# Kernel optimization log

Measured on AMD Instinct MI355X. Metric: run time of the kernel, lower is better.

The kernel has to match this reference:

```python
import jax, jax.numpy as jnp
import numpy as np

B, S, C = 4, 2048, 2048
D = C // 4  # head dim = 512

def setup_inputs() -> dict:
    key = jax.random.key(0)
    k1, k2, k3, k4, k5 = jax.random.split(key, 5)
    scale = 1.0 / np.sqrt(C)
    return {
        "x": jax.random.normal(k1, (B, S, C), dtype=jnp.float32),
        "Wqkv": jax.random.normal(k2, (3 * D, C), dtype=jnp.float32) * scale,
        "bqkv": jax.random.normal(k3, (3 * D,), dtype=jnp.float32) * 0.01,
        "Wo": jax.random.normal(k4, (C, D), dtype=jnp.float32) * (1.0 / np.sqrt(D)),
        "bo": jax.random.normal(k5, (C,), dtype=jnp.float32) * 0.01,
    }

def reference(x, Wqkv, bqkv, Wo, bo):
    Bx, Sx, Cx = x.shape
    d = Cx // 4
    # fused QKV projection: [B,S,3d] -> split into q,k,v each [B,S,d]
    qkv = jnp.einsum('bsc,oc->bso', x, Wqkv) + bqkv
    qkv = qkv.reshape(Bx, Sx, 3, d)
    q, k, v = qkv[:, :, 0], qkv[:, :, 1], qkv[:, :, 2]
    # scaled dot-product attention (full [B,S,S] scores, as in original)
    attn = jnp.einsum('bqd,bkd->bqk', q, k) / jnp.sqrt(jnp.asarray(d, x.dtype))
    attn = jax.nn.softmax(attn, axis=-1)
    ctx = jnp.einsum('bqk,bkd->bqd', attn, v)
    # output projection d -> C
    return jnp.einsum('bsd,od->bso', ctx, Wo) + bo
```

## Files before the change

kernel.cpp:

```cpp
#include <hip/hip_runtime.h>
#include <math.h>


typedef __bf16 bf16;
typedef bf16 bf16x8 __attribute__((ext_vector_type(8)));
typedef bf16 bf16x4 __attribute__((ext_vector_type(4)));
typedef float f32x4 __attribute__((ext_vector_type(4)));

#define BB 4
#define SS 2048
#define CC 2048
#define DD 512
#define ND3 1536
#define MM 8192

typedef const __attribute__((address_space(1))) unsigned int g_u32;
typedef __attribute__((address_space(3))) unsigned int l_u32;

__device__ __forceinline__ void gl_lds16(const bf16* g, bf16* l) {
    __builtin_amdgcn_global_load_lds((g_u32*)g, (l_u32*)l, 16, 0, 0);
}

#define N4_X   (MM * CC / 4)
#define N4_WQ  (ND3 * CC / 4)
#define N4_WO  (CC * DD / 4)
#define N4_RS  (MM / 4)
#define N4_TOT (N4_X + N4_WQ + N4_WO + N4_RS)

__global__ __launch_bounds__(256) void prep(const float* __restrict__ x,
                                            const float* __restrict__ Wqkv,
                                            const float* __restrict__ Wo,
                                            bf16* __restrict__ xb,
                                            bf16* __restrict__ wqkvb,
                                            bf16* __restrict__ wob,
                                            float* __restrict__ rsum) {
    int i = blockIdx.x * 256 + threadIdx.x;
    const int stride = gridDim.x * 256;
    for (; i < N4_TOT; i += stride) {
        if (i < N4_X + N4_WQ + N4_WO) {
            const float* src; bf16* dst; int j = i;
            if (j < N4_X)                { src = x;    dst = xb; }
            else if (j < N4_X + N4_WQ)   { src = Wqkv; dst = wqkvb; j -= N4_X; }
            else                         { src = Wo;   dst = wob;   j -= N4_X + N4_WQ; }
            float4 v = ((const float4*)src)[j];
            bf16x4 o;
            o[0] = (bf16)v.x; o[1] = (bf16)v.y; o[2] = (bf16)v.z; o[3] = (bf16)v.w;
            ((bf16x4*)dst)[j] = o;
        } else {
            int j = i - (N4_X + N4_WQ + N4_WO);
            ((float4*)rsum)[j] = float4{0.f, 0.f, 0.f, 0.f};
        }
    }
}

#define SLOT_E 16384
#define CH_B   8192

template <bool OUT_BF16, int EPI>
__device__ __forceinline__ void gemm256_body(const bf16* __restrict__ A,
                                             const bf16* __restrict__ Bm,
                                             const float* __restrict__ bias,
                                             float* __restrict__ rowsum,
                                             bf16* __restrict__ vTp,
                                             void* __restrict__ Cv,
                                             int K, int lda, int ldb, int ldc,
                                             long ab, long bb, long cb,
                                             float scale) {
    extern __shared__ bf16 lds[];
    A  += (size_t)blockIdx.z * ab;
    Bm += (size_t)blockIdx.z * bb;
    const int m0 = blockIdx.y * 256, n0 = blockIdx.x * 256;
    const int t = threadIdx.x, lane = t & 63, w = t >> 6;
    const int wm = (w >> 2) * 128, wn = (w & 3) * 64;
    const int cl = lane & 15, q = lane >> 4;
    const int swzr = (q ^ ((cl >> 1) & 3)) * 8;
    const int srow = t >> 2;
    const int swz  = (t & 3) ^ ((t >> 3) & 3);
    const bf16* pa = A  + (size_t)(m0 + srow) * lda + swz * 8;
    const bf16* pb = Bm + (size_t)(n0 + srow) * ldb + swz * 8;
    bf16* lw = lds + w * 512;

    f32x4 acc[8][4] = {};
    const int NC = K >> 5;

    auto STAGE = [&](int j) {
        bf16* s = lw + (j & 3) * SLOT_E;
        const bf16* ga = pa + j * 32;
        const bf16* gb = pb + j * 32;
        gl_lds16(ga,                     s);
        gl_lds16(ga + (size_t)128 * lda, s + 4096);
        gl_lds16(gb,                     s + CH_B);
        gl_lds16(gb + (size_t)128 * ldb, s + CH_B + 4096);
    };
    auto FRAGS = [&](int j, bf16x8 (&af)[8], bf16x8 (&bfr)[4]) {
        const bf16* sa = lds + (j & 3) * SLOT_E + (wm + cl) * 32 + swzr;
        const bf16* sb = lds + (j & 3) * SLOT_E + CH_B + (wn + cl) * 32 + swzr;
#pragma unroll
        for (int i = 0; i < 8; i++)  af[i]  = *(const bf16x8*)(sa + i * 512);
#pragma unroll
        for (int jj = 0; jj < 4; jj++) bfr[jj] = *(const bf16x8*)(sb + jj * 512);
    };
    auto MFMAS = [&](bf16x8 (&af)[8], bf16x8 (&bfr)[4]) {
        __builtin_amdgcn_s_setprio(1);
#pragma unroll
        for (int i = 0; i < 8; i++)
#pragma unroll
            for (int jj = 0; jj < 4; jj++)
                acc[i][jj] = __builtin_amdgcn_mfma_f32_16x16x32_bf16(
                                 af[i], bfr[jj], acc[i][jj], 0, 0, 0);
        __builtin_amdgcn_s_setprio(0);
    };

    STAGE(0); STAGE(1); STAGE(2);
    asm volatile("s_waitcnt vmcnt(8)" ::: "memory");
    __builtin_amdgcn_s_barrier();

    for (int j = 0; j < NC - 3; ++j) {
        bf16x8 af[8], bfr[4];
        FRAGS(j, af, bfr);
        STAGE(j + 3);
        MFMAS(af, bfr);
        asm volatile("s_waitcnt vmcnt(8)" ::: "memory");
        __builtin_amdgcn_s_barrier();
    }
    {   bf16x8 af[8], bfr[4];
        FRAGS(NC - 3, af, bfr); MFMAS(af, bfr);
        asm volatile("s_waitcnt vmcnt(4)" ::: "memory");
        __builtin_amdgcn_s_barrier();
    }
    {   bf16x8 af[8], bfr[4];
        FRAGS(NC - 2, af, bfr); MFMAS(af, bfr);
        asm volatile("s_waitcnt vmcnt(0)" ::: "memory");
        __builtin_amdgcn_s_barrier();
    }
    {   bf16x8 af[8], bfr[4];
        FRAGS(NC - 1, af, bfr); MFMAS(af, bfr);
    }

    if constexpr (EPI == 4) {
        float cs[4] = {0.f, 0.f, 0.f, 0.f};
#pragma unroll
        for (int i = 0; i < 8; i++)
#pragma unroll
            for (int jj = 0; jj < 4; jj++) {
                int col = n0 + wn + jj * 16 + cl;
                int row = m0 + wm + i * 16 + q * 4;
                bf16x4 o;
#pragma unroll
                for (int r = 0; r < 4; r++) {
                    float e = __expf(acc[i][jj][r] * scale);
                    cs[jj] += e;
                    o[r] = (bf16)e;
                }
                *(bf16x4*)&((bf16*)Cv)[(size_t)blockIdx.z * cb + (size_t)col * ldc + row] = o;
            }
#pragma unroll
        for (int jj = 0; jj < 4; jj++) {
            cs[jj] += __shfl_xor(cs[jj], 16, 64);
            cs[jj] += __shfl_xor(cs[jj], 32, 64);
        }
        if (q == 0) {
#pragma unroll
            for (int jj = 0; jj < 4; jj++)
                atomicAdd(&rowsum[(size_t)blockIdx.z * SS + n0 + wn + jj * 16 + cl], cs[jj]);
        }
        return;
    }

    const bool v_block = (EPI == 3) && (n0 >= 1024);
#pragma unroll
    for (int i = 0; i < 8; i++) {
#pragma unroll
        for (int jj = 0; jj < 4; jj++) {
            int col = n0 + wn + jj * 16 + cl;
            float bvv = bias ? bias[col] : 0.0f;
            if (v_block) {
                int row = m0 + wm + i * 16 + q * 4;
                int b = row >> 11, s = row & 2047;
                bf16x4 o;
#pragma unroll
                for (int r = 0; r < 4; r++) o[r] = (bf16)(acc[i][jj][r] * scale + bvv);
                *(bf16x4*)&vTp[((size_t)b * DD + (col - 1024)) * SS + s] = o;
            } else {
#pragma unroll
                for (int r = 0; r < 4; r++) {
                    int row = m0 + wm + i * 16 + q * 4 + r;
                    float val = acc[i][jj][r] * scale + bvv;
                    if (OUT_BF16)
                        ((bf16*)Cv)[(size_t)blockIdx.z * cb + (size_t)row * ldc + col] = (bf16)val;
                    else
                        ((float*)Cv)[(size_t)blockIdx.z * cb + (size_t)row * ldc + col] = val;
                }
            }
        }
    }
}

template <bool OUT_BF16, int BN, int EPI>
__device__ __forceinline__ void gemm_body(const bf16* __restrict__ A,
                                          const bf16* __restrict__ Bm,
                                          const float* __restrict__ bias,
                                          float* __restrict__ rowsum,
                                          bf16* __restrict__ vTp,
                                          void* __restrict__ Cv,
                                          int K, int lda, int ldb, int ldc,
                                          long ab, long bb, long cb,
                                          float scale) {
    constexpr int TM = (BN == 128) ? 4 : 2;
    constexpr int NB = (BN == 128) ? 4 : 2;
    __shared__ bf16 As[128 * 64];
    __shared__ bf16 Bs[BN * 64];
    A += (size_t)blockIdx.z * ab;
    Bm += (size_t)blockIdx.z * bb;
    const int m0 = blockIdx.y * 128, n0 = blockIdx.x * BN;
    const int t = threadIdx.x, lane = t & 63, w = t >> 6;
    const int wm = (BN == 128) ? (w >> 1) * 64 : w * 32;
    const int wn = (BN == 128) ? (w & 1) * 64 : 0;
    const int q = lane >> 4, cl = lane & 15;
    const int srow = lane >> 3;
    const int sblk = (lane & 7) ^ srow;
    const int scol = sblk * 8;
    const bf16* pa = A + (size_t)(m0 + w * 32 + srow) * lda + scol;
    const int brow0 = (BN == 128) ? w * 32 : w * 16;
    const bf16* pb = Bm + (size_t)(n0 + brow0 + srow) * ldb + scol;
    bf16* lA = As + (w * 32) * 64;
    bf16* lB = Bs + brow0 * 64;
    const int rblk0 = (q ^ (cl & 7)) * 8;
    const int rblk1 = ((4 + q) ^ (cl & 7)) * 8;

    f32x4 acc[TM][4] = {};
    for (int k0 = 0; k0 < K; k0 += 64) {
#pragma unroll
        for (int n = 0; n < 4; n++)
            gl_lds16(pa + k0 + (size_t)(n * 8) * lda, lA + n * 8 * 64);
#pragma unroll
        for (int n = 0; n < NB; n++)
            gl_lds16(pb + k0 + (size_t)(n * 8) * ldb, lB + n * 8 * 64);
        __syncthreads();
#pragma unroll
        for (int h = 0; h < 2; h++) {
            const int rb = h ? rblk1 : rblk0;
            bf16x8 af[TM], bfr[4];
#pragma unroll
            for (int i = 0; i < TM; i++)
                af[i] = *(const bf16x8*)&As[(wm + i * 16 + cl) * 64 + rb];
#pragma unroll
            for (int j = 0; j < 4; j++)
                bfr[j] = *(const bf16x8*)&Bs[(wn + j * 16 + cl) * 64 + rb];
#pragma unroll
            for (int i = 0; i < TM; i++)
#pragma unroll
                for (int j = 0; j < 4; j++)
                    acc[i][j] = __builtin_amdgcn_mfma_f32_16x16x32_bf16(af[i], bfr[j], acc[i][j], 0, 0, 0);
        }
        __syncthreads();
    }

    if constexpr (EPI == 4 || EPI == 5) {
        float inv[4], cs[4] = {0.f, 0.f, 0.f, 0.f};
        if constexpr (EPI == 5) {
#pragma unroll
            for (int j = 0; j < 4; j++)
                inv[j] = 1.0f / rowsum[(size_t)blockIdx.z * SS + n0 + wn + j * 16 + cl];
        }
#pragma unroll
        for (int i = 0; i < TM; i++)
#pragma unroll
            for (int j = 0; j < 4; j++) {
                int col = n0 + wn + j * 16 + cl;
                int row = m0 + wm + i * 16 + q * 4;
                bf16x4 o;
                if constexpr (EPI == 4) {
#pragma unroll
                    for (int r = 0; r < 4; r++) {
                        float e = __expf(acc[i][j][r] * scale);
                        cs[j] += e;
                        o[r] = (bf16)e;
                    }
                } else {
#pragma unroll
                    for (int r = 0; r < 4; r++) o[r] = (bf16)(acc[i][j][r] * inv[j]);
                }
                *(bf16x4*)&((bf16*)Cv)[(size_t)blockIdx.z * cb + (size_t)col * ldc + row] = o;
            }
        if constexpr (EPI == 4) {
#pragma unroll
            for (int j = 0; j < 4; j++) {
                cs[j] += __shfl_xor(cs[j], 16, 64);
                cs[j] += __shfl_xor(cs[j], 32, 64);
            }
            if (q == 0) {
#pragma unroll
                for (int j = 0; j < 4; j++)
                    atomicAdd(&rowsum[(size_t)blockIdx.z * SS + n0 + wn + j * 16 + cl], cs[j]);
            }
        }
        return;
    }
}

__global__ __launch_bounds__(512, 2) void k_qkv(const bf16* A, const bf16* Bm,
        const float* bias, bf16* vTp, void* Cv, int K, int lda, int ldb, int ldc,
        float scale) {
    gemm256_body<true, 3>(A, Bm, bias, nullptr, vTp, Cv, K, lda, ldb, ldc, 0, 0, 0, scale);
}
__global__ __launch_bounds__(512, 2) void k_score(const bf16* A, const bf16* Bm,
        float* rowsum, void* Cv, int K, int lda, int ldb, int ldc,
        long ab, long bb, long cb, float scale) {
    gemm256_body<true, 4>(A, Bm, nullptr, rowsum, nullptr, Cv, K, lda, ldb, ldc, ab, bb, cb, scale);
}
__global__ __launch_bounds__(256) void k_pv(const bf16* A, const bf16* Bm,
        float* rowsum, void* Cv, int K, int lda, int ldb, int ldc,
        long ab, long bb, long cb, float scale) {
    gemm_body<true, 64, 5>(A, Bm, nullptr, rowsum, nullptr, Cv, K, lda, ldb, ldc, ab, bb, cb, scale);
}
__global__ __launch_bounds__(512, 2) void k_out(const bf16* A, const bf16* Bm,
        const float* bias, void* Cv, int K, int lda, int ldb, int ldc,
        float scale) {
    gemm256_body<false, 0>(A, Bm, bias, nullptr, nullptr, Cv, K, lda, ldb, ldc, 0, 0, 0, scale);
}

extern "C" void kernel_launch(void* const* d_in, const int* in_sizes, int n_in,
                              void* d_out, int out_size, void* d_ws, size_t ws_size,
                              hipStream_t stream) {
    const float* x    = (const float*)d_in[0];
    const float* Wqkv = (const float*)d_in[1];
    const float* bqkv = (const float*)d_in[2];
    const float* Wo   = (const float*)d_in[3];
    const float* bo   = (const float*)d_in[4];
    float* out = (float*)d_out;

    char* ws = (char*)d_ws;
    size_t off = 0;
    bf16* xb    = (bf16*)(ws + off); off += (size_t)MM * CC * 2;
    bf16* wqkvb = (bf16*)(ws + off); off += (size_t)ND3 * CC * 2;
    bf16* wob   = (bf16*)(ws + off); off += (size_t)CC * DD * 2;
    bf16* qkvb  = (bf16*)(ws + off); off += (size_t)MM * ND3 * 2;
    bf16* vT    = (bf16*)(ws + off); off += (size_t)BB * DD * SS * 2;
    bf16* expS  = (bf16*)(ws + off); off += (size_t)BB * SS * SS * 2;
    bf16* ctxb  = (bf16*)(ws + off); off += (size_t)MM * DD * 2;
    float* rsum = (float*)(ws + off); off += (size_t)MM * 4;

    static int lds_attr_set = 0;
    if (!lds_attr_set) {
        hipFuncSetAttribute((const void*)k_qkv,
                            hipFuncAttributeMaxDynamicSharedMemorySize, 131072);
        hipFuncSetAttribute((const void*)k_score,
                            hipFuncAttributeMaxDynamicSharedMemorySize, 131072);
        hipFuncSetAttribute((const void*)k_out,
                            hipFuncAttributeMaxDynamicSharedMemorySize, 131072);
        lds_attr_set = 1;
    }

    prep<<<2048, 256, 0, stream>>>(x, Wqkv, Wo, xb, wqkvb, wob, rsum);

    k_qkv<<<dim3(ND3 / 256, MM / 256, 1), 512, 131072, stream>>>(
        xb, wqkvb, bqkv, vT, qkvb, CC, CC, CC, ND3, 1.0f);

    k_score<<<dim3(SS / 256, SS / 256, BB), 512, 131072, stream>>>(
        qkvb + 512 , qkvb , rsum, expS,
        DD, ND3, ND3, SS,
        (long)SS * ND3, (long)SS * ND3, (long)SS * SS,
        0.044194173824159216f );

    k_pv<<<dim3(SS / 64, DD / 128, BB), 256, 0, stream>>>(
        vT, expS, rsum, ctxb,
        SS, SS, SS, DD,
        (long)DD * SS, (long)SS * SS, (long)SS * DD, 1.0f);

    k_out<<<dim3(CC / 256, MM / 256, 1), 512, 131072, stream>>>(
        ctxb, wob, bo, out, DD, DD, DD, CC, 1.0f);

    (void)in_sizes; (void)n_in; (void)out_size; (void)ws_size;
}
```

Baseline: 283.2 us.

## Split GEMM k-chunk into two half-phases interleaving LDS reads, staging and MFMAs

Each 32-wide k-chunk of the 256x256 GEMM main loop now runs in two half-phases. Each phase reads half of the A fragments from LDS, issues half of the global-to-LDS staging (A or B tile), and then runs 16 MFMAs, with extra workgroup barriers and lgkmcnt waits around each phase. The goal is to lower register pressure (4 A fragments live instead of 8) and to interleave memory traffic with MFMA work in a ping-pong style schedule. The cost is two extra barriers per chunk, which may add stalls.

```diff
diff --git a/kernel.cpp b/kernel.cpp
--- a/kernel.cpp
+++ b/kernel.cpp
@@ -55,6 +55,38 @@
 
 #define SLOT_E 16384
 #define CH_B   8192
+
+#define CHUNK_BODY(j, DO_STAGE)                                               \
+    {                                                                         \
+        const bf16* sa = lds + ((j) & 3) * SLOT_E + (wm + cl) * 32 + swzr;    \
+        const bf16* sb = lds + ((j) & 3) * SLOT_E + CH_B + (wn + cl) * 32 + swzr; \
+        bf16x8 af[4], bfr[4];                                                 \
+        _Pragma("unroll") for (int i = 0; i < 4; i++)                         \
+            af[i] = *(const bf16x8*)(sa + i * 512);                           \
+        _Pragma("unroll") for (int jj = 0; jj < 4; jj++)                      \
+            bfr[jj] = *(const bf16x8*)(sb + jj * 512);                        \
+        if (DO_STAGE) STAGE_A((j) + 3);                                       \
+        __builtin_amdgcn_s_barrier();                                         \
+        asm volatile("s_waitcnt lgkmcnt(0)" ::: "memory");                    \
+        __builtin_amdgcn_s_setprio(1);                                        \
+        _Pragma("unroll") for (int i = 0; i < 4; i++)                         \
+            _Pragma("unroll") for (int jj = 0; jj < 4; jj++)                  \
+                acc[i][jj] = __builtin_amdgcn_mfma_f32_16x16x32_bf16(         \
+                                 af[i], bfr[jj], acc[i][jj], 0, 0, 0);        \
+        __builtin_amdgcn_s_setprio(0);                                        \
+        __builtin_amdgcn_s_barrier();                                         \
+        _Pragma("unroll") for (int i = 0; i < 4; i++)                         \
+            af[i] = *(const bf16x8*)(sa + (4 + i) * 512);                     \
+        if (DO_STAGE) STAGE_B((j) + 3);                                       \
+        __builtin_amdgcn_s_barrier();                                         \
+        asm volatile("s_waitcnt lgkmcnt(0)" ::: "memory");                    \
+        __builtin_amdgcn_s_setprio(1);                                        \
+        _Pragma("unroll") for (int i = 0; i < 4; i++)                         \
+            _Pragma("unroll") for (int jj = 0; jj < 4; jj++)                  \
+                acc[4 + i][jj] = __builtin_amdgcn_mfma_f32_16x16x32_bf16(     \
+                                 af[i], bfr[jj], acc[4 + i][jj], 0, 0, 0);    \
+        __builtin_amdgcn_s_setprio(0);                                        \
+    }
 
 template <bool OUT_BF16, int EPI>
 __device__ __forceinline__ void gemm256_body(const bf16* __restrict__ A,
@@ -83,59 +115,37 @@
     f32x4 acc[8][4] = {};
     const int NC = K >> 5;
 
-    auto STAGE = [&](int j) {
+    auto STAGE_A = [&](int j) {
         bf16* s = lw + (j & 3) * SLOT_E;
         const bf16* ga = pa + j * 32;
-        const bf16* gb = pb + j * 32;
         gl_lds16(ga,                     s);
         gl_lds16(ga + (size_t)128 * lda, s + 4096);
-        gl_lds16(gb,                     s + CH_B);
-        gl_lds16(gb + (size_t)128 * ldb, s + CH_B + 4096);
     };
-    auto FRAGS = [&](int j, bf16x8 (&af)[8], bf16x8 (&bfr)[4]) {
-        const bf16* sa = lds + (j & 3) * SLOT_E + (wm + cl) * 32 + swzr;
-        const bf16* sb = lds + (j & 3) * SLOT_E + CH_B + (wn + cl) * 32 + swzr;
-#pragma unroll
-        for (int i = 0; i < 8; i++)  af[i]  = *(const bf16x8*)(sa + i * 512);
-#pragma unroll
-        for (int jj = 0; jj < 4; jj++) bfr[jj] = *(const bf16x8*)(sb + jj * 512);
+    auto STAGE_B = [&](int j) {
+        bf16* s = lw + (j & 3) * SLOT_E + CH_B;
+        const bf16* gb = pb + j * 32;
+        gl_lds16(gb,                     s);
+        gl_lds16(gb + (size_t)128 * ldb, s + 4096);
     };
-    auto MFMAS = [&](bf16x8 (&af)[8], bf16x8 (&bfr)[4]) {
-        __builtin_amdgcn_s_setprio(1);
-#pragma unroll
-        for (int i = 0; i < 8; i++)
-#pragma unroll
-            for (int jj = 0; jj < 4; jj++)
-                acc[i][jj] = __builtin_amdgcn_mfma_f32_16x16x32_bf16(
-                                 af[i], bfr[jj], acc[i][jj], 0, 0, 0);
-        __builtin_amdgcn_s_setprio(0);
-    };
-
-    STAGE(0); STAGE(1); STAGE(2);
+
+    STAGE_A(0); STAGE_B(0);
+    STAGE_A(1); STAGE_B(1);
+    STAGE_A(2); STAGE_B(2);
     asm volatile("s_waitcnt vmcnt(8)" ::: "memory");
     __builtin_amdgcn_s_barrier();
 
     for (int j = 0; j < NC - 3; ++j) {
-        bf16x8 af[8], bfr[4];
-        FRAGS(j, af, bfr);
-        STAGE(j + 3);
-        MFMAS(af, bfr);
+        CHUNK_BODY(j, true);
         asm volatile("s_waitcnt vmcnt(8)" ::: "memory");
         __builtin_amdgcn_s_barrier();
     }
-    {   bf16x8 af[8], bfr[4];
-        FRAGS(NC - 3, af, bfr); MFMAS(af, bfr);
-        asm volatile("s_waitcnt vmcnt(4)" ::: "memory");
-        __builtin_amdgcn_s_barrier();
-    }
-    {   bf16x8 af[8], bfr[4];
-        FRAGS(NC - 2, af, bfr); MFMAS(af, bfr);
-        asm volatile("s_waitcnt vmcnt(0)" ::: "memory");
-        __builtin_amdgcn_s_barrier();
-    }
-    {   bf16x8 af[8], bfr[4];
-        FRAGS(NC - 1, af, bfr); MFMAS(af, bfr);
-    }
+    CHUNK_BODY(NC - 3, false);
+    asm volatile("s_waitcnt vmcnt(4)" ::: "memory");
+    __builtin_amdgcn_s_barrier();
+    CHUNK_BODY(NC - 2, false);
+    asm volatile("s_waitcnt vmcnt(0)" ::: "memory");
+    __builtin_amdgcn_s_barrier();
+    CHUNK_BODY(NC - 1, false);
 
     if constexpr (EPI == 4) {
         float cs[4] = {0.f, 0.f, 0.f, 0.f};
```

After: 284.9 us. No clear change (+0.6%).

## Specialize QKV GEMM with 256x192 tiles and A-fragment double buffering

Applied to the files above, without the earlier changes.

Replaces the generic 256x256 QKV projection kernel with a dedicated kernel using 256x192 tiles. The grid grows from 6x32 to 8x32 blocks, so more CUs are covered, and each stage uses less LDS. It also prefetches the next chunk's A fragments into registers while the current MFMAs run, adding an lgkmcnt wait before each barrier. Dead epilogue branches are removed from the generic bodies. The costs are higher register pressure from two A fragment sets and uneven B loads, since only half the waves load the second B half.

```diff
diff --git a/kernel.cpp b/kernel.cpp
--- a/kernel.cpp
+++ b/kernel.cpp
@@ -20,6 +20,10 @@
 __device__ __forceinline__ void gl_lds16(const bf16* g, bf16* l) {
     __builtin_amdgcn_global_load_lds((g_u32*)g, (l_u32*)l, 16, 0, 0);
 }
+
+#define VMW(n) asm volatile("s_waitcnt vmcnt(" #n ")" ::: "memory")
+#define LKW0   asm volatile("s_waitcnt lgkmcnt(0)" ::: "memory")
+#define BAR    __builtin_amdgcn_s_barrier()
 
 #define N4_X   (MM * CC / 4)
 #define N4_WQ  (ND3 * CC / 4)
@@ -53,6 +57,105 @@
     }
 }
 
+#define SLOT3_E 14336
+
+__global__ __launch_bounds__(512, 2) void k_qkv(const bf16* __restrict__ A,
+        const bf16* __restrict__ Bm, const float* __restrict__ bias,
+        bf16* __restrict__ vTp, bf16* __restrict__ Cv,
+        int K, int lda, int ldb, int ldc) {
+    extern __shared__ bf16 lds[];
+    const int m0 = blockIdx.y * 256, n0 = blockIdx.x * 192;
+    const int t = threadIdx.x, lane = t & 63, w = t >> 6;
+    const int wm = (w >> 2) * 128, wn = (w & 3) * 48;
+    const int cl = lane & 15, q = lane >> 4;
+    const int swzr = (q ^ ((cl >> 1) & 3)) * 8;
+    const int srow = t >> 2;
+    const int swz  = (t & 3) ^ ((t >> 3) & 3);
+    const bf16* pa = A  + (size_t)(m0 + srow) * lda + swz * 8;
+    const bf16* pb = Bm + (size_t)(n0 + srow) * ldb + swz * 8;
+    bf16* lw = lds + w * 512;
+
+    f32x4 acc[8][3] = {};
+    const int NC = K >> 5;
+
+    auto STAGE = [&](int j) {
+        bf16* s = lw + (j & 3) * SLOT3_E;
+        const bf16* ga = pa + j * 32;
+        const bf16* gb = pb + j * 32;
+        gl_lds16(ga,                     s);
+        gl_lds16(ga + (size_t)128 * lda, s + 4096);
+        gl_lds16(gb,                     s + 8192);
+        if (w < 4) gl_lds16(gb + (size_t)128 * ldb, s + 8192 + 4096);
+    };
+    auto FRAGS_A = [&](int j, bf16x8 (&fa)[8]) {
+        const bf16* sa = lds + (j & 3) * SLOT3_E + (wm + cl) * 32 + swzr;
+#pragma unroll
+        for (int i = 0; i < 8; i++) fa[i] = *(const bf16x8*)(sa + i * 512);
+    };
+    auto FRAGS_B = [&](int j, bf16x8 (&fb)[3]) {
+        const bf16* sb = lds + (j & 3) * SLOT3_E + 8192 + (wn + cl) * 32 + swzr;
+#pragma unroll
+        for (int jj = 0; jj < 3; jj++) fb[jj] = *(const bf16x8*)(sb + jj * 512);
+    };
+    auto MFMAS3 = [&](bf16x8 (&fa)[8], bf16x8 (&fb)[3]) {
+        __builtin_amdgcn_s_setprio(1);
+#pragma unroll
+        for (int i = 0; i < 8; i++)
+#pragma unroll
+            for (int jj = 0; jj < 3; jj++)
+                acc[i][jj] = __builtin_amdgcn_mfma_f32_16x16x32_bf16(
+                                 fa[i], fb[jj], acc[i][jj], 0, 0, 0);
+        __builtin_amdgcn_s_setprio(0);
+    };
+
+#define QCHUNK(j, FCUR, FNXT, DO_NEXT, DO_STAGE)                              \
+    {                                                                         \
+        bf16x8 fb[3];                                                         \
+        FRAGS_B((j), fb);                                                     \
+        if (DO_NEXT) FRAGS_A((j) + 1, FNXT);                                  \
+        if (DO_STAGE) STAGE((j) + 3);                                         \
+        MFMAS3(FCUR, fb);                                                     \
+    }
+
+    STAGE(0); STAGE(1); STAGE(2);
+    VMW(4); BAR;
+    bf16x8 fa0[8], fa1[8];
+    FRAGS_A(0, fa0);
+    for (int j = 0; j < NC - 4; j += 2) {
+        QCHUNK(j,     fa0, fa1, true, true);  VMW(4); LKW0; BAR;
+        QCHUNK(j + 1, fa1, fa0, true, true);  VMW(4); LKW0; BAR;
+    }
+    QCHUNK(NC - 4, fa0, fa1, true, true);   VMW(4); LKW0; BAR;
+    QCHUNK(NC - 3, fa1, fa0, true, false);  VMW(0); LKW0; BAR;
+    QCHUNK(NC - 2, fa0, fa1, true, false);  LKW0; BAR;
+    QCHUNK(NC - 1, fa1, fa0, false, false);
+#undef QCHUNK
+
+#pragma unroll
+    for (int i = 0; i < 8; i++) {
+#pragma unroll
+        for (int jj = 0; jj < 3; jj++) {
+            int colg = n0 + wn + jj * 16;
+            int col = colg + cl;
+            float bvv = bias[col];
+            if (colg >= 1024) {
+                int row = m0 + wm + i * 16 + q * 4;
+                int b = row >> 11, s = row & 2047;
+                bf16x4 o;
+#pragma unroll
+                for (int r = 0; r < 4; r++) o[r] = (bf16)(acc[i][jj][r] + bvv);
+                *(bf16x4*)&vTp[((size_t)b * DD + (col - 1024)) * SS + s] = o;
+            } else {
+#pragma unroll
+                for (int r = 0; r < 4; r++) {
+                    int row = m0 + wm + i * 16 + q * 4 + r;
+                    Cv[(size_t)row * ldc + col] = (bf16)(acc[i][jj][r] + bvv);
+                }
+            }
+        }
+    }
+}
+
 #define SLOT_E 16384
 #define CH_B   8192
 
@@ -61,7 +164,6 @@
                                              const bf16* __restrict__ Bm,
                                              const float* __restrict__ bias,
                                              float* __restrict__ rowsum,
-                                             bf16* __restrict__ vTp,
                                              void* __restrict__ Cv,
                                              int K, int lda, int ldb, int ldc,
                                              long ab, long bb, long cb,
@@ -112,26 +214,22 @@
     };
 
     STAGE(0); STAGE(1); STAGE(2);
-    asm volatile("s_waitcnt vmcnt(8)" ::: "memory");
-    __builtin_amdgcn_s_barrier();
+    VMW(8); BAR;
 
     for (int j = 0; j < NC - 3; ++j) {
         bf16x8 af[8], bfr[4];
         FRAGS(j, af, bfr);
         STAGE(j + 3);
         MFMAS(af, bfr);
-        asm volatile("s_waitcnt vmcnt(8)" ::: "memory");
-        __builtin_amdgcn_s_barrier();
+        VMW(8); BAR;
     }
     {   bf16x8 af[8], bfr[4];
         FRAGS(NC - 3, af, bfr); MFMAS(af, bfr);
-        asm volatile("s_waitcnt vmcnt(4)" ::: "memory");
-        __builtin_amdgcn_s_barrier();
+        VMW(4); BAR;
     }
     {   bf16x8 af[8], bfr[4];
         FRAGS(NC - 2, af, bfr); MFMAS(af, bfr);
-        asm volatile("s_waitcnt vmcnt(0)" ::: "memory");
-        __builtin_amdgcn_s_barrier();
+        VMW(0); BAR;
     }
     {   bf16x8 af[8], bfr[4];
         FRAGS(NC - 1, af, bfr); MFMAS(af, bfr);
@@ -167,45 +265,32 @@
         return;
     }
 
-    const bool v_block = (EPI == 3) && (n0 >= 1024);
 #pragma unroll
     for (int i = 0; i < 8; i++) {
 #pragma unroll
         for (int jj = 0; jj < 4; jj++) {
             int col = n0 + wn + jj * 16 + cl;
             float bvv = bias ? bias[col] : 0.0f;
-            if (v_block) {
-                int row = m0 + wm + i * 16 + q * 4;
-                int b = row >> 11, s = row & 2047;
-                bf16x4 o;
-#pragma unroll
-                for (int r = 0; r < 4; r++) o[r] = (bf16)(acc[i][jj][r] * scale + bvv);
-                *(bf16x4*)&vTp[((size_t)b * DD + (col - 1024)) * SS + s] = o;
-            } else {
-#pragma unroll
-                for (int r = 0; r < 4; r++) {
-                    int row = m0 + wm + i * 16 + q * 4 + r;
-                    float val = acc[i][jj][r] * scale + bvv;
-                    if (OUT_BF16)
-                        ((bf16*)Cv)[(size_t)blockIdx.z * cb + (size_t)row * ldc + col] = (bf16)val;
-                    else
-                        ((float*)Cv)[(size_t)blockIdx.z * cb + (size_t)row * ldc + col] = val;
-                }
+#pragma unroll
+            for (int r = 0; r < 4; r++) {
+                int row = m0 + wm + i * 16 + q * 4 + r;
+                float val = acc[i][jj][r] * scale + bvv;
+                if (OUT_BF16)
+                    ((bf16*)Cv)[(size_t)blockIdx.z * cb + (size_t)row * ldc + col] = (bf16)val;
+                else
+                    ((float*)Cv)[(size_t)blockIdx.z * cb + (size_t)row * ldc + col] = val;
             }
         }
     }
 }
 
-template <bool OUT_BF16, int BN, int EPI>
+template <int BN, int EPI>
 __device__ __forceinline__ void gemm_body(const bf16* __restrict__ A,
                                           const bf16* __restrict__ Bm,
-                                          const float* __restrict__ bias,
                                           float* __restrict__ rowsum,
-                                          bf16* __restrict__ vTp,
                                           void* __restrict__ Cv,
                                           int K, int lda, int ldb, int ldc,
-                                          long ab, long bb, long cb,
-                                          float scale) {
+                                          long ab, long bb, long cb) {
     constexpr int TM = (BN == 128) ? 4 : 2;
     constexpr int NB = (BN == 128) ? 4 : 2;
     __shared__ bf16 As[128 * 64];
@@ -256,68 +341,37 @@
         __syncthreads();
     }
 
-    if constexpr (EPI == 4 || EPI == 5) {
-        float inv[4], cs[4] = {0.f, 0.f, 0.f, 0.f};
-        if constexpr (EPI == 5) {
-#pragma unroll
-            for (int j = 0; j < 4; j++)
-                inv[j] = 1.0f / rowsum[(size_t)blockIdx.z * SS + n0 + wn + j * 16 + cl];
-        }
-#pragma unroll
-        for (int i = 0; i < TM; i++)
-#pragma unroll
-            for (int j = 0; j < 4; j++) {
-                int col = n0 + wn + j * 16 + cl;
-                int row = m0 + wm + i * 16 + q * 4;
-                bf16x4 o;
-                if constexpr (EPI == 4) {
-#pragma unroll
-                    for (int r = 0; r < 4; r++) {
-                        float e = __expf(acc[i][j][r] * scale);
-                        cs[j] += e;
-                        o[r] = (bf16)e;
-                    }
-                } else {
-#pragma unroll
-                    for (int r = 0; r < 4; r++) o[r] = (bf16)(acc[i][j][r] * inv[j]);
-                }
-                *(bf16x4*)&((bf16*)Cv)[(size_t)blockIdx.z * cb + (size_t)col * ldc + row] = o;
-            }
-        if constexpr (EPI == 4) {
-#pragma unroll
-            for (int j = 0; j < 4; j++) {
-                cs[j] += __shfl_xor(cs[j], 16, 64);
-                cs[j] += __shfl_xor(cs[j], 32, 64);
-            }
-            if (q == 0) {
-#pragma unroll
-                for (int j = 0; j < 4; j++)
-                    atomicAdd(&rowsum[(size_t)blockIdx.z * SS + n0 + wn + j * 16 + cl], cs[j]);
-            }
-        }
-        return;
-    }
-}
-
-__global__ __launch_bounds__(512, 2) void k_qkv(const bf16* A, const bf16* Bm,
-        const float* bias, bf16* vTp, void* Cv, int K, int lda, int ldb, int ldc,
-        float scale) {
-    gemm256_body<true, 3>(A, Bm, bias, nullptr, vTp, Cv, K, lda, ldb, ldc, 0, 0, 0, scale);
-}
+    float inv[4];
+#pragma unroll
+    for (int j = 0; j < 4; j++)
+        inv[j] = 1.0f / rowsum[(size_t)blockIdx.z * SS + n0 + wn + j * 16 + cl];
+#pragma unroll
+    for (int i = 0; i < TM; i++)
+#pragma unroll
+        for (int j = 0; j < 4; j++) {
+            int col = n0 + wn + j * 16 + cl;
+            int row = m0 + wm + i * 16 + q * 4;
+            bf16x4 o;
+#pragma unroll
+            for (int r = 0; r < 4; r++) o[r] = (bf16)(acc[i][j][r] * inv[j]);
+            *(bf16x4*)&((bf16*)Cv)[(size_t)blockIdx.z * cb + (size_t)col * ldc + row] = o;
+        }
+}
+
 __global__ __launch_bounds__(512, 2) void k_score(const bf16* A, const bf16* Bm,
         float* rowsum, void* Cv, int K, int lda, int ldb, int ldc,
         long ab, long bb, long cb, float scale) {
-    gemm256_body<true, 4>(A, Bm, nullptr, rowsum, nullptr, Cv, K, lda, ldb, ldc, ab, bb, cb, scale);
+    gemm256_body<true, 4>(A, Bm, nullptr, rowsum, Cv, K, lda, ldb, ldc, ab, bb, cb, scale);
 }
 __global__ __launch_bounds__(256) void k_pv(const bf16* A, const bf16* Bm,
         float* rowsum, void* Cv, int K, int lda, int ldb, int ldc,
-        long ab, long bb, long cb, float scale) {
-    gemm_body<true, 64, 5>(A, Bm, nullptr, rowsum, nullptr, Cv, K, lda, ldb, ldc, ab, bb, cb, scale);
+        long ab, long bb, long cb) {
+    gemm_body<64, 5>(A, Bm, rowsum, Cv, K, lda, ldb, ldc, ab, bb, cb);
 }
 __global__ __launch_bounds__(512, 2) void k_out(const bf16* A, const bf16* Bm,
         const float* bias, void* Cv, int K, int lda, int ldb, int ldc,
         float scale) {
-    gemm256_body<false, 0>(A, Bm, bias, nullptr, nullptr, Cv, K, lda, ldb, ldc, 0, 0, 0, scale);
+    gemm256_body<false, 0>(A, Bm, bias, nullptr, Cv, K, lda, ldb, ldc, 0, 0, 0, scale);
 }
 
 extern "C" void kernel_launch(void* const* d_in, const int* in_sizes, int n_in,
@@ -354,8 +408,8 @@
 
     prep<<<2048, 256, 0, stream>>>(x, Wqkv, Wo, xb, wqkvb, wob, rsum);
 
-    k_qkv<<<dim3(ND3 / 256, MM / 256, 1), 512, 131072, stream>>>(
-        xb, wqkvb, bqkv, vT, qkvb, CC, CC, CC, ND3, 1.0f);
+    k_qkv<<<dim3(ND3 / 192, MM / 256, 1), 512, 4 * SLOT3_E * 2, stream>>>(
+        xb, wqkvb, bqkv, vT, qkvb, CC, CC, CC, ND3);
 
     k_score<<<dim3(SS / 256, SS / 256, BB), 512, 131072, stream>>>(
         qkvb + 512 , qkvb , rsum, expS,
@@ -366,7 +420,7 @@
     k_pv<<<dim3(SS / 64, DD / 128, BB), 256, 0, stream>>>(
         vT, expS, rsum, ctxb,
         SS, SS, SS, DD,
-        (long)DD * SS, (long)SS * SS, (long)SS * DD, 1.0f);
+        (long)DD * SS, (long)SS * SS, (long)SS * DD);
 
     k_out<<<dim3(CC / 256, MM / 256, 1), 512, 131072, stream>>>(
         ctxb, wob, bo, out, DD, DD, DD, CC, 1.0f);
```

Measured after the change: 269.7 us. 1.05x faster.

## Store exp-scores row-major and compute PV with 128x128 tiles

Applied to the files above, without the earlier changes.

The score kernel now computes S = Q·K^T, so exp-scores are stored row-major (query rows) instead of transposed. Row sums are reduced across lanes with shuffles, then accumulated atomically per query row. The PV kernel becomes a dedicated 128x128-tile GEMM of expS times vT, normalizing by per-row inverse sums in the epilogue. The aim is larger PV tiles with more reuse and fewer blocks, at the cost of scalar bf16 stores instead of bf16x4 vector stores in both epilogues.

```diff
diff --git a/kernel.cpp b/kernel.cpp
--- a/kernel.cpp
+++ b/kernel.cpp
@@ -20,6 +20,9 @@
 __device__ __forceinline__ void gl_lds16(const bf16* g, bf16* l) {
     __builtin_amdgcn_global_load_lds((g_u32*)g, (l_u32*)l, 16, 0, 0);
 }
+
+#define VMW(n) asm volatile("s_waitcnt vmcnt(" #n ")" ::: "memory")
+#define BAR    __builtin_amdgcn_s_barrier()
 
 #define N4_X   (MM * CC / 4)
 #define N4_WQ  (ND3 * CC / 4)
@@ -112,57 +115,58 @@
     };
 
     STAGE(0); STAGE(1); STAGE(2);
-    asm volatile("s_waitcnt vmcnt(8)" ::: "memory");
-    __builtin_amdgcn_s_barrier();
+    VMW(8); BAR;
 
     for (int j = 0; j < NC - 3; ++j) {
         bf16x8 af[8], bfr[4];
         FRAGS(j, af, bfr);
         STAGE(j + 3);
         MFMAS(af, bfr);
-        asm volatile("s_waitcnt vmcnt(8)" ::: "memory");
-        __builtin_amdgcn_s_barrier();
+        VMW(8); BAR;
     }
     {   bf16x8 af[8], bfr[4];
         FRAGS(NC - 3, af, bfr); MFMAS(af, bfr);
-        asm volatile("s_waitcnt vmcnt(4)" ::: "memory");
-        __builtin_amdgcn_s_barrier();
+        VMW(4); BAR;
     }
     {   bf16x8 af[8], bfr[4];
         FRAGS(NC - 2, af, bfr); MFMAS(af, bfr);
-        asm volatile("s_waitcnt vmcnt(0)" ::: "memory");
-        __builtin_amdgcn_s_barrier();
+        VMW(0); BAR;
     }
     {   bf16x8 af[8], bfr[4];
         FRAGS(NC - 1, af, bfr); MFMAS(af, bfr);
     }
 
-    if constexpr (EPI == 4) {
-        float cs[4] = {0.f, 0.f, 0.f, 0.f};
-#pragma unroll
-        for (int i = 0; i < 8; i++)
+    if constexpr (EPI == 7) {
+#pragma unroll
+        for (int i = 0; i < 8; i++) {
+            float ex[4][4];
+#pragma unroll
+            for (int jj = 0; jj < 4; jj++)
+#pragma unroll
+                for (int r = 0; r < 4; r++)
+                    ex[jj][r] = __expf(acc[i][jj][r] * scale);
 #pragma unroll
             for (int jj = 0; jj < 4; jj++) {
                 int col = n0 + wn + jj * 16 + cl;
-                int row = m0 + wm + i * 16 + q * 4;
-                bf16x4 o;
 #pragma unroll
                 for (int r = 0; r < 4; r++) {
-                    float e = __expf(acc[i][jj][r] * scale);
-                    cs[jj] += e;
-                    o[r] = (bf16)e;
+                    int row = m0 + wm + i * 16 + q * 4 + r;
+                    ((bf16*)Cv)[(size_t)blockIdx.z * cb + (size_t)row * ldc + col] =
+                        (bf16)ex[jj][r];
                 }
-                *(bf16x4*)&((bf16*)Cv)[(size_t)blockIdx.z * cb + (size_t)col * ldc + row] = o;
             }
 #pragma unroll
-        for (int jj = 0; jj < 4; jj++) {
-            cs[jj] += __shfl_xor(cs[jj], 16, 64);
-            cs[jj] += __shfl_xor(cs[jj], 32, 64);
-        }
-        if (q == 0) {
-#pragma unroll
-            for (int jj = 0; jj < 4; jj++)
-                atomicAdd(&rowsum[(size_t)blockIdx.z * SS + n0 + wn + jj * 16 + cl], cs[jj]);
+            for (int r = 0; r < 4; r++) {
+                float rs = ex[0][r] + ex[1][r] + ex[2][r] + ex[3][r];
+                rs += __shfl_xor(rs, 1, 64);
+                rs += __shfl_xor(rs, 2, 64);
+                rs += __shfl_xor(rs, 4, 64);
+                rs += __shfl_xor(rs, 8, 64);
+                if (cl == 0) {
+                    int row = m0 + wm + i * 16 + q * 4 + r;
+                    atomicAdd(&rowsum[(size_t)blockIdx.z * SS + row], rs);
+                }
+            }
         }
         return;
     }
@@ -196,59 +200,49 @@
     }
 }
 
-template <bool OUT_BF16, int BN, int EPI>
-__device__ __forceinline__ void gemm_body(const bf16* __restrict__ A,
-                                          const bf16* __restrict__ Bm,
-                                          const float* __restrict__ bias,
-                                          float* __restrict__ rowsum,
-                                          bf16* __restrict__ vTp,
-                                          void* __restrict__ Cv,
-                                          int K, int lda, int ldb, int ldc,
-                                          long ab, long bb, long cb,
-                                          float scale) {
-    constexpr int TM = (BN == 128) ? 4 : 2;
-    constexpr int NB = (BN == 128) ? 4 : 2;
+__global__ __launch_bounds__(256) void k_pv(const bf16* __restrict__ A,
+        const bf16* __restrict__ Bm, float* __restrict__ rowsum,
+        bf16* __restrict__ Cv, int K, int lda, int ldb, int ldc,
+        long ab, long bb, long cb) {
     __shared__ bf16 As[128 * 64];
-    __shared__ bf16 Bs[BN * 64];
+    __shared__ bf16 Bs[128 * 64];
     A += (size_t)blockIdx.z * ab;
     Bm += (size_t)blockIdx.z * bb;
-    const int m0 = blockIdx.y * 128, n0 = blockIdx.x * BN;
+    const int m0 = blockIdx.y * 128, n0 = blockIdx.x * 128;
     const int t = threadIdx.x, lane = t & 63, w = t >> 6;
-    const int wm = (BN == 128) ? (w >> 1) * 64 : w * 32;
-    const int wn = (BN == 128) ? (w & 1) * 64 : 0;
+    const int wm = (w >> 1) * 64, wn = (w & 1) * 64;
     const int q = lane >> 4, cl = lane & 15;
     const int srow = lane >> 3;
     const int sblk = (lane & 7) ^ srow;
     const int scol = sblk * 8;
     const bf16* pa = A + (size_t)(m0 + w * 32 + srow) * lda + scol;
-    const int brow0 = (BN == 128) ? w * 32 : w * 16;
-    const bf16* pb = Bm + (size_t)(n0 + brow0 + srow) * ldb + scol;
+    const bf16* pb = Bm + (size_t)(n0 + w * 32 + srow) * ldb + scol;
     bf16* lA = As + (w * 32) * 64;
-    bf16* lB = Bs + brow0 * 64;
+    bf16* lB = Bs + (w * 32) * 64;
     const int rblk0 = (q ^ (cl & 7)) * 8;
     const int rblk1 = ((4 + q) ^ (cl & 7)) * 8;
 
-    f32x4 acc[TM][4] = {};
+    f32x4 acc[4][4] = {};
     for (int k0 = 0; k0 < K; k0 += 64) {
 #pragma unroll
         for (int n = 0; n < 4; n++)
             gl_lds16(pa + k0 + (size_t)(n * 8) * lda, lA + n * 8 * 64);
 #pragma unroll
-        for (int n = 0; n < NB; n++)
+        for (int n = 0; n < 4; n++)
             gl_lds16(pb + k0 + (size_t)(n * 8) * ldb, lB + n * 8 * 64);
         __syncthreads();
 #pragma unroll
         for (int h = 0; h < 2; h++) {
             const int rb = h ? rblk1 : rblk0;
-            bf16x8 af[TM], bfr[4];
-#pragma unroll
-            for (int i = 0; i < TM; i++)
+            bf16x8 af[4], bfr[4];
+#pragma unroll
+            for (int i = 0; i < 4; i++)
                 af[i] = *(const bf16x8*)&As[(wm + i * 16 + cl) * 64 + rb];
 #pragma unroll
             for (int j = 0; j < 4; j++)
                 bfr[j] = *(const bf16x8*)&Bs[(wn + j * 16 + cl) * 64 + rb];
 #pragma unroll
-            for (int i = 0; i < TM; i++)
+            for (int i = 0; i < 4; i++)
 #pragma unroll
                 for (int j = 0; j < 4; j++)
                     acc[i][j] = __builtin_amdgcn_mfma_f32_16x16x32_bf16(af[i], bfr[j], acc[i][j], 0, 0, 0);
@@ -256,47 +250,24 @@
         __syncthreads();
     }
 
-    if constexpr (EPI == 4 || EPI == 5) {
-        float inv[4], cs[4] = {0.f, 0.f, 0.f, 0.f};
-        if constexpr (EPI == 5) {
-#pragma unroll
-            for (int j = 0; j < 4; j++)
-                inv[j] = 1.0f / rowsum[(size_t)blockIdx.z * SS + n0 + wn + j * 16 + cl];
-        }
-#pragma unroll
-        for (int i = 0; i < TM; i++)
-#pragma unroll
-            for (int j = 0; j < 4; j++) {
-                int col = n0 + wn + j * 16 + cl;
-                int row = m0 + wm + i * 16 + q * 4;
-                bf16x4 o;
-                if constexpr (EPI == 4) {
-#pragma unroll
-                    for (int r = 0; r < 4; r++) {
-                        float e = __expf(acc[i][j][r] * scale);
-                        cs[j] += e;
-                        o[r] = (bf16)e;
-                    }
-                } else {
-#pragma unroll
-                    for (int r = 0; r < 4; r++) o[r] = (bf16)(acc[i][j][r] * inv[j]);
-                }
-                *(bf16x4*)&((bf16*)Cv)[(size_t)blockIdx.z * cb + (size_t)col * ldc + row] = o;
+    float inv[4][4];
+#pragma unroll
+    for (int i = 0; i < 4; i++)
+#pragma unroll
+        for (int r = 0; r < 4; r++)
+            inv[i][r] = 1.0f / rowsum[(size_t)blockIdx.z * SS + m0 + wm + i * 16 + q * 4 + r];
+#pragma unroll
+    for (int i = 0; i < 4; i++)
+#pragma unroll
+        for (int j = 0; j < 4; j++) {
+            int col = n0 + wn + j * 16 + cl;
+#pragma unroll
+            for (int r = 0; r < 4; r++) {
+                int row = m0 + wm + i * 16 + q * 4 + r;
+                Cv[(size_t)blockIdx.z * cb + (size_t)row * ldc + col] =
+                    (bf16)(acc[i][j][r] * inv[i][r]);
             }
-        if constexpr (EPI == 4) {
-#pragma unroll
-            for (int j = 0; j < 4; j++) {
-                cs[j] += __shfl_xor(cs[j], 16, 64);
-                cs[j] += __shfl_xor(cs[j], 32, 64);
-            }
-            if (q == 0) {
-#pragma unroll
-                for (int j = 0; j < 4; j++)
-                    atomicAdd(&rowsum[(size_t)blockIdx.z * SS + n0 + wn + j * 16 + cl], cs[j]);
-            }
-        }
-        return;
-    }
+        }
 }
 
 __global__ __launch_bounds__(512, 2) void k_qkv(const bf16* A, const bf16* Bm,
@@ -307,12 +278,7 @@
 __global__ __launch_bounds__(512, 2) void k_score(const bf16* A, const bf16* Bm,
         float* rowsum, void* Cv, int K, int lda, int ldb, int ldc,
         long ab, long bb, long cb, float scale) {
-    gemm256_body<true, 4>(A, Bm, nullptr, rowsum, nullptr, Cv, K, lda, ldb, ldc, ab, bb, cb, scale);
-}
-__global__ __launch_bounds__(256) void k_pv(const bf16* A, const bf16* Bm,
-        float* rowsum, void* Cv, int K, int lda, int ldb, int ldc,
-        long ab, long bb, long cb, float scale) {
-    gemm_body<true, 64, 5>(A, Bm, nullptr, rowsum, nullptr, Cv, K, lda, ldb, ldc, ab, bb, cb, scale);
+    gemm256_body<true, 7>(A, Bm, nullptr, rowsum, nullptr, Cv, K, lda, ldb, ldc, ab, bb, cb, scale);
 }
 __global__ __launch_bounds__(512, 2) void k_out(const bf16* A, const bf16* Bm,
         const float* bias, void* Cv, int K, int lda, int ldb, int ldc,
@@ -358,15 +324,15 @@
         xb, wqkvb, bqkv, vT, qkvb, CC, CC, CC, ND3, 1.0f);
 
     k_score<<<dim3(SS / 256, SS / 256, BB), 512, 131072, stream>>>(
-        qkvb + 512 , qkvb , rsum, expS,
+        qkvb , qkvb + 512 , rsum, expS,
         DD, ND3, ND3, SS,
         (long)SS * ND3, (long)SS * ND3, (long)SS * SS,
         0.044194173824159216f );
 
-    k_pv<<<dim3(SS / 64, DD / 128, BB), 256, 0, stream>>>(
-        vT, expS, rsum, ctxb,
+    k_pv<<<dim3(DD / 128, SS / 128, BB), 256, 0, stream>>>(
+        expS, vT, rsum, ctxb,
         SS, SS, SS, DD,
-        (long)DD * SS, (long)SS * SS, (long)SS * DD, 1.0f);
+        (long)SS * SS, (long)DD * SS, (long)SS * DD);
 
     k_out<<<dim3(CC / 256, MM / 256, 1), 512, 131072, stream>>>(
         ctxb, wob, bo, out, DD, DD, DD, CC, 1.0f);
```

Result: slower. 294.3 us (+3.9%).
